# Performance work log

Hardware: AMD Instinct MI355X
Metric: run time of the kernel (lower is better)

## Reference

```python
import jax, jax.numpy as jnp
import numpy as np

B, C, H, W = 8, 256, 64, 64
NH = 8
CM = 2048
EPS = 1e-5


def setup_inputs() -> dict:
    key = jax.random.key(0)
    ks = jax.random.split(key, 16)
    n = lambda k, s: (jax.random.normal(k, s, dtype=jnp.float32) * 0.02)
    return {
        'x': jax.random.normal(ks[0], (B, C, H, W), dtype=jnp.float32),
        'Wqkv': n(ks[1], (C, 3 * C)), 'bqkv': n(ks[2], (3 * C,)),
        'dw_w': n(ks[3], (C, 1, 3, 3)), 'dw_b': n(ks[4], (C,)),
        'Wproj': n(ks[5], (C, C)), 'bproj': n(ks[6], (C,)),
        'bn1_g': jnp.ones((C,), jnp.float32), 'bn1_b': jnp.zeros((C,), jnp.float32),
        'bn1_m': n(ks[7], (C,)), 'bn1_v': jax.random.uniform(ks[8], (C,), dtype=jnp.float32) + 0.5,
        'alpha1': jnp.ones((1,), jnp.float32),
        'Wfc1': n(ks[9], (C, CM)), 'bfc1': n(ks[10], (CM,)),
        'Wfc2': n(ks[11], (CM, C)), 'bfc2': n(ks[12], (C,)),
        'bn2_g': jnp.ones((C,), jnp.float32), 'bn2_b': jnp.zeros((C,), jnp.float32),
        'bn2_m': n(ks[13], (C,)), 'bn2_v': jax.random.uniform(ks[14], (C,), dtype=jnp.float32) + 0.5,
        'alpha2': jnp.ones((1,), jnp.float32),
    }


def _repbn(x, g, b, m, v, alpha):
    # eval-mode RepBN: BatchNorm1d with running stats over channel dim + alpha*x
    bn = (x - m) * jax.lax.rsqrt(v + EPS) * g + b
    return bn + alpha * x


def reference(x, Wqkv, bqkv, dw_w, dw_b, Wproj, bproj,
              bn1_g, bn1_b, bn1_m, bn1_v, alpha1,
              Wfc1, bfc1, Wfc2, bfc2,
              bn2_g, bn2_b, bn2_m, bn2_v, alpha2):
    b, c, h, w = x.shape
    n = h * w
    hd = c // NH
    scale = hd ** (-0.5)
    t = x.reshape(b, c, n).transpose(0, 2, 1)  # [B,N,C]

    # --- SimplifiedLinearAttention ---
    qkv = (t @ Wqkv + bqkv).reshape(b, n, 3, NH, hd).transpose(2, 0, 3, 1, 4)
    q, k, v = qkv[0], qkv[1], qkv[2]          # [B,H,N,hd]
    q = jax.nn.relu(q) * scale
    k = jax.nn.relu(k)
    ctx = jnp.einsum('bhnd,bhne->bhde', k, v)  # [B,H,hd,hd] small context
    out = jnp.einsum('bhnd,bhde->bhne', q, ctx)
    out = out.transpose(0, 2, 1, 3).reshape(b, n, c)
    img = out.transpose(0, 2, 1).reshape(b, c, h, w)
    img = jax.lax.conv_general_dilated(img, dw_w, (1, 1), 'SAME',
                                       feature_group_count=c)
    img = img + dw_b[None, :, None, None]
    out = img.reshape(b, c, n).transpose(0, 2, 1)
    out = out @ Wproj + bproj

    # residual + RepBN (eval branch of LinearNorm)
    t = _repbn(t + out, bn1_g, bn1_b, bn1_m, bn1_v, alpha1)

    # FFN (exact GELU as nn.GELU default)
    ff = jax.nn.gelu(t @ Wfc1 + bfc1, approximate=False) @ Wfc2 + bfc2
    t = _repbn(t + ff, bn2_g, bn2_b, bn2_m, bn2_v, alpha2)

    return t.transpose(0, 2, 1).reshape(b, c, h, w)
```

## Files before the change

### kernel.cpp

```cpp
#include <hip/hip_runtime.h>
#include <hip/hip_bf16.h>
#include <math.h>

constexpr int B_ = 8, C_ = 256, H_ = 64, W_ = 64;
constexpr int N_ = H_ * W_;
constexpr int NH_ = 8;
constexpr int CM_ = 2048;
constexpr int M_ = B_ * N_;
constexpr float EPS_ = 1e-5f;

typedef __bf16 bf16_t;
typedef bf16_t bf16x4 __attribute__((ext_vector_type(4)));
typedef bf16_t bf16x8 __attribute__((ext_vector_type(8)));
typedef float f32x4 __attribute__((ext_vector_type(4)));

__device__ inline bf16_t f2b(float f) {
    __hip_bfloat16 h = __float2bfloat16(f);
    return *reinterpret_cast<bf16_t*>(&h);
}
__device__ inline float b2f(bf16_t b) {
    unsigned short u = *reinterpret_cast<unsigned short*>(&b);
    unsigned int x = (unsigned int)u << 16;
    return *reinterpret_cast<float*>(&x);
}
__device__ inline float gelu_ap(float y) {
    float u = y * (0.7978845608f + 0.0356774081f * y * y);
    float e = __expf(2.0f * u);
    return y - y * __builtin_amdgcn_rcpf(e + 1.0f);
}

#define GLOAD_LDS16(gptr, lptr)                                                     \
    __builtin_amdgcn_global_load_lds(                                               \
        (const __attribute__((address_space(1))) void*)(gptr),                      \
        (__attribute__((address_space(3))) void*)(lptr), 16, 0, 0)

template <int MODE>
__global__ void transpose_cast(const void* __restrict__ in_, bf16_t* __restrict__ outb) {
    __shared__ float tile[32][33];
    int b  = blockIdx.z;
    int n0 = blockIdx.x * 32;
    int c0 = blockIdx.y * 32;
    int tx = threadIdx.x, ty = threadIdx.y;
#pragma unroll
    for (int i = ty; i < 32; i += 8) {
        size_t off = (size_t)b * C_ * N_ + (size_t)(c0 + i) * N_ + n0 + tx;
        tile[i][tx] = (MODE == 0) ? ((const float*)in_)[off] : b2f(((const bf16_t*)in_)[off]);
    }
    __syncthreads();
#pragma unroll
    for (int i = ty; i < 32; i += 8) {
        size_t off = (size_t)b * N_ * C_ + (size_t)(n0 + i) * C_ + c0 + tx;
        outb[off] = f2b(tile[tx][i]);
    }
}

__global__ void wcastT(const float* __restrict__ W, bf16_t* __restrict__ Wt,
                       int K, int N) {
    __shared__ float tile[32][33];
    int k0 = blockIdx.y * 32, n0 = blockIdx.x * 32;
    int tx = threadIdx.x, ty = threadIdx.y;
#pragma unroll
    for (int i = ty; i < 32; i += 8)
        tile[i][tx] = W[(size_t)(k0 + i) * N + n0 + tx];
    __syncthreads();
#pragma unroll
    for (int i = ty; i < 32; i += 8)
        Wt[(size_t)(n0 + i) * K + k0 + tx] = f2b(tile[tx][i]);
}

template <int EPI>
__global__ __launch_bounds__(256)
void gemm_swp(const bf16_t* __restrict__ Wt, const bf16_t* __restrict__ Act,
              const float* __restrict__ bias, bf16_t* __restrict__ Cb,
              int M, int N, int K,
              const bf16_t* __restrict__ tres_b,
              const float* __restrict__ g, const float* __restrict__ bb,
              const float* __restrict__ mm, const float* __restrict__ vv,
              const float* __restrict__ alpha) {
    __shared__ bf16x8 ldsv[2048];
    char* lds = (char*)ldsv;

    int tid  = threadIdx.x;
    int lane = tid & 63;
    int w    = tid >> 6;
    int wi   = w >> 1, wj = w & 1;

    int nwg = gridDim.x * gridDim.y;
    int bid = blockIdx.y * gridDim.x + blockIdx.x;
    int swz = (bid & 7) * (nwg >> 3) + (bid >> 3);
    int bx = swz % gridDim.x, by = swz / gridDim.x;
    int bch = bx * 128, bm = by * 128;

    int rowl = lane & 15, kq = lane >> 4;

    f32x4 acc[4][4] = {};

    for (int k0 = 0; k0 < K; k0 += 64) {
#pragma unroll
        for (int j = 0; j < 4; ++j) {
            int jj = w * 4 + j;
            int msub = jj >> 1, kh = jj & 1;
            const bf16_t* gw = Wt + ((size_t)(bch + msub * 16 + rowl) * K + k0 + kh * 32 + kq * 8);
            GLOAD_LDS16(gw, lds + jj * 1024);
            const bf16_t* ga = Act + ((size_t)(bm + msub * 16 + rowl) * K + k0 + kh * 32 + kq * 8);
            GLOAD_LDS16(ga, lds + 16384 + jj * 1024);
        }
        __syncthreads();
#pragma unroll
        for (int ks = 0; ks < 2; ++ks) {
            bf16x8 wf[4], af[4];
#pragma unroll
            for (int i = 0; i < 4; ++i) wf[i] = ldsv[((wi * 4 + i) * 2 + ks) * 64 + lane];
#pragma unroll
            for (int j = 0; j < 4; ++j) af[j] = ldsv[1024 + ((wj * 4 + j) * 2 + ks) * 64 + lane];
#pragma unroll
            for (int i = 0; i < 4; ++i)
#pragma unroll
                for (int j = 0; j < 4; ++j)
                    acc[i][j] = __builtin_amdgcn_mfma_f32_16x16x32_bf16(wf[i], af[j], acc[i][j], 0, 0, 0);
        }
        __syncthreads();
    }

    float alpha_v = (EPI == 1) ? alpha[0] : 0.f;
#pragma unroll
    for (int i = 0; i < 4; ++i) {
        int ch = bch + wi * 64 + i * 16 + (lane >> 4) * 4;
        f32x4 b4 = *(const f32x4*)(bias + ch);
        f32x4 rs4, B4, m4;
        if (EPI == 1) {
            f32x4 g4 = *(const f32x4*)(g + ch);
            f32x4 v4 = *(const f32x4*)(vv + ch);
            B4 = *(const f32x4*)(bb + ch);
            m4 = *(const f32x4*)(mm + ch);
#pragma unroll
            for (int r = 0; r < 4; ++r) rs4[r] = rsqrtf(v4[r] + EPS_) * g4[r];
        }
#pragma unroll
        for (int j = 0; j < 4; ++j) {
            int m = bm + wj * 64 + j * 16 + (lane & 15);
            f32x4 a = acc[i][j];
            bf16_t ob[4];
            if (EPI == 4) {
#pragma unroll
                for (int r = 0; r < 4; ++r) ob[r] = f2b(a[r] + b4[r]);
            } else if (EPI == 2) {
#pragma unroll
                for (int r = 0; r < 4; ++r) ob[r] = f2b(gelu_ap(a[r] + b4[r]));
            } else {
                bf16x4 t4 = *(const bf16x4*)(tres_b + (size_t)m * N + ch);
#pragma unroll
                for (int r = 0; r < 4; ++r) {
                    float z = b2f(t4[r]) + a[r] + b4[r];
                    ob[r] = f2b((z - m4[r]) * rs4[r] + B4[r] + alpha_v * z);
                }
            }
            *(bf16x4*)(Cb + (size_t)m * N + ch) = *(bf16x4*)ob;
        }
    }
}

__global__ __launch_bounds__(256)
void gemm_bf16(const bf16_t* __restrict__ A, const bf16_t* __restrict__ Bt,
               const float* __restrict__ bias,
               float* __restrict__ Cf,
               int M, int N, int K,
               const bf16_t* __restrict__ tres_b,
               const float* __restrict__ g, const float* __restrict__ bb,
               const float* __restrict__ mm, const float* __restrict__ vv,
               const float* __restrict__ alpha) {
    __shared__ bf16x8 ldsv[2048];
    char* lds = (char*)ldsv;

    int tid  = threadIdx.x;
    int lane = tid & 63;
    int w    = tid >> 6;
    int wm   = w >> 1, wn = w & 1;

    int nwg = gridDim.x * gridDim.y;
    int bid = blockIdx.y * gridDim.x + blockIdx.x;
    int swz = (bid & 7) * (nwg >> 3) + (bid >> 3);
    int bx = swz % gridDim.x, by = swz / gridDim.x;
    int brow = by * 128, bcol = bx * 128;

    int rowl = lane & 15, kq = lane >> 4;

    f32x4 acc[4][4] = {};

    for (int k0 = 0; k0 < K; k0 += 64) {
#pragma unroll
        for (int j = 0; j < 4; ++j) {
            int jj = w * 4 + j;
            int msub = jj >> 1, kh = jj & 1;
            const bf16_t* ga = A + ((size_t)(brow + msub * 16 + rowl) * K + k0 + kh * 32 + kq * 8);
            GLOAD_LDS16(ga, lds + jj * 1024);
            const bf16_t* gb = Bt + ((size_t)(bcol + msub * 16 + rowl) * K + k0 + kh * 32 + kq * 8);
            GLOAD_LDS16(gb, lds + 16384 + jj * 1024);
        }
        __syncthreads();
#pragma unroll
        for (int ks = 0; ks < 2; ++ks) {
            bf16x8 af[4], bfr[4];
#pragma unroll
            for (int m = 0; m < 4; ++m) af[m] = ldsv[((wm * 4 + m) * 2 + ks) * 64 + lane];
#pragma unroll
            for (int n = 0; n < 4; ++n) bfr[n] = ldsv[1024 + ((wn * 4 + n) * 2 + ks) * 64 + lane];
#pragma unroll
            for (int m = 0; m < 4; ++m)
#pragma unroll
                for (int n = 0; n < 4; ++n)
                    acc[m][n] = __builtin_amdgcn_mfma_f32_16x16x32_bf16(af[m], bfr[n], acc[m][n], 0, 0, 0);
        }
        __syncthreads();
    }

    float alpha_v = alpha[0];
#pragma unroll
    for (int m = 0; m < 4; ++m) {
        int mbase = brow + wm * 64 + m * 16 + (lane >> 4) * 4;
        int bi = mbase >> 12, ni = mbase & (N_ - 1);
#pragma unroll
        for (int n = 0; n < 4; ++n) {
            int col = bcol + wn * 64 + n * 16 + (lane & 15);
            float bv = bias[col];
            float rs = rsqrtf(vv[col] + EPS_) * g[col];
            float bbv = bb[col], mv = mm[col];
            f32x4 o4;
#pragma unroll
            for (int r = 0; r < 4; ++r) {
                float z = b2f(tres_b[(size_t)(mbase + r) * C_ + col]) + acc[m][n][r] + bv;
                o4[r] = (z - mv) * rs + bbv + alpha_v * z;
            }
            *(f32x4*)(Cf + ((size_t)bi * C_ + col) * N_ + ni) = o4;
        }
    }
}

__global__ void ctx_partial(const bf16_t* __restrict__ qkv, float* __restrict__ ctxp) {
    __shared__ float kb[64][40];
    __shared__ float vb[64][40];
    int seg = blockIdx.x;
    int bh  = blockIdx.y;
    int b = bh >> 3, h = bh & 7;
    int tid = threadIdx.x;
    int d  = tid >> 3;
    int e0 = (tid & 7) * 4;
    int lrow = tid >> 2, lcol = (tid & 3) * 8;
    float acc[4] = {0.f, 0.f, 0.f, 0.f};
    const size_t base = (size_t)b * N_ * 768 + h * 32;
    for (int n0 = seg * 512; n0 < seg * 512 + 512; n0 += 64) {
        size_t ra = base + (size_t)(n0 + lrow) * 768 + lcol;
        bf16x8 kv8 = *(const bf16x8*)(qkv + ra + 256);
        bf16x8 vv8 = *(const bf16x8*)(qkv + ra + 512);
#pragma unroll
        for (int j = 0; j < 8; ++j) {
            kb[lrow][lcol + j] = b2f(kv8[j]);
            vb[lrow][lcol + j] = b2f(vv8[j]);
        }
        __syncthreads();
#pragma unroll
        for (int nl = 0; nl < 64; ++nl) {
            float kv = fmaxf(kb[nl][d], 0.f);
#pragma unroll
            for (int j = 0; j < 4; ++j)
                acc[j] = fmaf(kv, vb[nl][e0 + j], acc[j]);
        }
        __syncthreads();
    }
    float* o = ctxp + ((size_t)seg * 64 + bh) * 1024 + d * 32 + e0;
#pragma unroll
    for (int j = 0; j < 4; ++j) o[j] = acc[j];
}

__global__ void ctx_reduce(const float* __restrict__ ctxp, float* __restrict__ ctx) {
    int idx = blockIdx.x * 256 + threadIdx.x;
    float s = 0.f;
#pragma unroll
    for (int seg = 0; seg < 8; ++seg) s += ctxp[(size_t)seg * 65536 + idx];
    ctx[idx] = s;
}

__global__ void attn_out(const bf16_t* __restrict__ qkv, const float* __restrict__ ctx,
                         bf16_t* __restrict__ img) {
    __shared__ float qb[64][33];
    __shared__ float cs[32][32];
    int n0 = blockIdx.x * 64;
    int bh = blockIdx.y;
    int b = bh >> 3, h = bh & 7;
    int tid = threadIdx.x;
    const float scale = 0.17677669529663687f;
    {
        float4 vv = ((const float4*)(ctx + (size_t)bh * 1024))[tid];
        ((float4*)&cs[0][0])[tid] = vv;
    }
    const size_t base = (size_t)b * N_ * 768 + h * 32;
    int lrow = tid >> 2, lcol = (tid & 3) * 8;
    {
        bf16x8 q8 = *(const bf16x8*)(qkv + base + (size_t)(n0 + lrow) * 768 + lcol);
#pragma unroll
        for (int j = 0; j < 8; ++j)
            qb[lrow][lcol + j] = fmaxf(b2f(q8[j]), 0.f) * scale;
    }
    __syncthreads();
    int nl = tid & 63, ebase = tid >> 6;
    bf16_t* outp = img + ((size_t)b * C_ + h * 32) * N_ + n0 + nl;
#pragma unroll
    for (int p = 0; p < 8; ++p) {
        int e = ebase + p * 4;
        float s = 0.f;
#pragma unroll
        for (int dd = 0; dd < 32; ++dd)
            s = fmaf(qb[nl][dd], cs[dd][e], s);
        outp[(size_t)e * N_] = f2b(s);
    }
}

__global__ __launch_bounds__(256)
void dwconv3x3(const bf16_t* __restrict__ img, const float* __restrict__ w,
               const float* __restrict__ bias, bf16_t* __restrict__ out) {
    __shared__ float sp[64][65];
    int bc = blockIdx.x;
    int c  = bc & 255;
    int tid = threadIdx.x;
    const bf16_t* ip = img + (size_t)bc * N_;
#pragma unroll
    for (int l = 0; l < 2; ++l) {
        int flat = (tid + l * 256) * 8;
        int row = flat >> 6, col = flat & 63;
        bf16x8 v8 = *(const bf16x8*)(ip + flat);
#pragma unroll
        for (int j = 0; j < 8; ++j) sp[row][col + j] = b2f(v8[j]);
    }
    float wv[9];
#pragma unroll
    for (int j = 0; j < 9; ++j) wv[j] = w[c * 9 + j];
    float bv = bias[c];
    __syncthreads();

    int y = tid >> 2, x0 = (tid & 3) * 16;
    float o[16];
#pragma unroll
    for (int i = 0; i < 16; ++i) o[i] = bv;
#pragma unroll
    for (int dy = -1; dy <= 1; ++dy) {
        int yy = y + dy;
        if (yy < 0 || yy > 63) continue;
#pragma unroll
        for (int dx = -1; dx <= 1; ++dx) {
            float wgt = wv[(dy + 1) * 3 + dx + 1];
#pragma unroll
            for (int i = 0; i < 16; ++i) {
                int xx = x0 + i + dx;
                float val = (xx < 0 || xx > 63) ? 0.f : sp[yy][xx];
                o[i] = fmaf(wgt, val, o[i]);
            }
        }
    }
    bf16_t ob[16];
#pragma unroll
    for (int i = 0; i < 16; ++i) ob[i] = f2b(o[i]);
    *(bf16x8*)(out + (size_t)bc * N_ + y * 64 + x0)     = *(bf16x8*)&ob[0];
    *(bf16x8*)(out + (size_t)bc * N_ + y * 64 + x0 + 8) = *(bf16x8*)&ob[8];
}

extern "C" void kernel_launch(void* const* d_in, const int* in_sizes, int n_in,
                              void* d_out, int out_size, void* d_ws, size_t ws_size,
                              hipStream_t stream) {
    const float* x     = (const float*)d_in[0];
    const float* Wqkv  = (const float*)d_in[1];
    const float* bqkv  = (const float*)d_in[2];
    const float* dw_w  = (const float*)d_in[3];
    const float* dw_b  = (const float*)d_in[4];
    const float* Wproj = (const float*)d_in[5];
    const float* bproj = (const float*)d_in[6];
    const float* bn1_g = (const float*)d_in[7];
    const float* bn1_b = (const float*)d_in[8];
    const float* bn1_m = (const float*)d_in[9];
    const float* bn1_v = (const float*)d_in[10];
    const float* alpha1= (const float*)d_in[11];
    const float* Wfc1  = (const float*)d_in[12];
    const float* bfc1  = (const float*)d_in[13];
    const float* Wfc2  = (const float*)d_in[14];
    const float* bfc2  = (const float*)d_in[15];
    const float* bn2_g = (const float*)d_in[16];
    const float* bn2_b = (const float*)d_in[17];
    const float* bn2_m = (const float*)d_in[18];
    const float* bn2_v = (const float*)d_in[19];
    const float* alpha2= (const float*)d_in[20];
    float* out = (float*)d_out;

    char* ws = (char*)d_ws;
    bf16_t* t_b2    = (bf16_t*)(ws);
    bf16_t* WqkvT   = (bf16_t*)(ws + 16777216);
    bf16_t* WprojT  = (bf16_t*)(ws + 17170432);
    bf16_t* Wfc1T   = (bf16_t*)(ws + 17301504);
    bf16_t* Wfc2T   = (bf16_t*)(ws + 18350080);
    float*  ctxp    = (float*)(ws + 19398656);
    float*  ctx     = (float*)(ws + 21495808);
    bf16_t* t_b     = (bf16_t*)(ws + 21757952);
    bf16_t* qkv_b   = (bf16_t*)(ws + 38535168);
    bf16_t* img_b   = (bf16_t*)(ws + 88866816);
    bf16_t* conv_b  = (bf16_t*)(ws + 105644032);
    bf16_t* convT_b = (bf16_t*)(ws + 122421248);
    bf16_t* hidden  = (bf16_t*)(ws + 21757952);

    transpose_cast<0><<<dim3(N_ / 32, C_ / 32, B_), dim3(32, 8), 0, stream>>>(x, t_b);
    wcastT<<<dim3(768 / 32, C_ / 32), dim3(32, 8), 0, stream>>>(Wqkv, WqkvT, C_, 768);
    wcastT<<<dim3(C_ / 32, C_ / 32), dim3(32, 8), 0, stream>>>(Wproj, WprojT, C_, C_);
    wcastT<<<dim3(CM_ / 32, C_ / 32), dim3(32, 8), 0, stream>>>(Wfc1, Wfc1T, C_, CM_);
    wcastT<<<dim3(C_ / 32, CM_ / 32), dim3(32, 8), 0, stream>>>(Wfc2, Wfc2T, CM_, C_);

    gemm_swp<4><<<dim3(768 / 128, M_ / 128), 256, 0, stream>>>(
        WqkvT, t_b, bqkv, qkv_b, M_, 768, C_,
        nullptr, nullptr, nullptr, nullptr, nullptr, nullptr);

    ctx_partial<<<dim3(8, B_ * NH_), 256, 0, stream>>>(qkv_b, ctxp);
    ctx_reduce<<<256, 256, 0, stream>>>(ctxp, ctx);

    attn_out<<<dim3(N_ / 64, B_ * NH_), 256, 0, stream>>>(qkv_b, ctx, img_b);

    dwconv3x3<<<B_ * C_, 256, 0, stream>>>(img_b, dw_w, dw_b, conv_b);

    transpose_cast<1><<<dim3(N_ / 32, C_ / 32, B_), dim3(32, 8), 0, stream>>>(conv_b, convT_b);

    gemm_swp<1><<<dim3(C_ / 128, M_ / 128), 256, 0, stream>>>(
        WprojT, convT_b, bproj, t_b2, M_, C_, C_,
        t_b, bn1_g, bn1_b, bn1_m, bn1_v, alpha1);

    gemm_swp<2><<<dim3(CM_ / 128, M_ / 128), 256, 0, stream>>>(
        Wfc1T, t_b2, bfc1, hidden, M_, CM_, C_,
        nullptr, nullptr, nullptr, nullptr, nullptr, nullptr);

    gemm_bf16<<<dim3(C_ / 128, M_ / 128), 256, 0, stream>>>(
        hidden, Wfc2T, bfc2, out, M_, C_, CM_,
        t_b2, bn2_g, bn2_b, bn2_m, bn2_v, alpha2);
}
```

Measured before the change: 338.0 us.

## Double-buffer LDS in GEMM kernels and merge prep casts into one launch

Both GEMM kernels now use two LDS buffers, issuing async global-to-LDS loads for the next K tile while the MFMAs run on the current one. This drops one barrier per iteration. The input transpose and the four weight transpose-casts are merged into a single launch to cut launch overhead. In exchange, LDS per block doubles to 64KB, which may lower occupancy.

```diff
diff --git a/kernel.cpp b/kernel.cpp
--- a/kernel.cpp
+++ b/kernel.cpp
@@ -34,38 +34,57 @@
         (const __attribute__((address_space(1))) void*)(gptr),                      \
         (__attribute__((address_space(3))) void*)(lptr), 16, 0, 0)
 
-template <int MODE>
-__global__ void transpose_cast(const void* __restrict__ in_, bf16_t* __restrict__ outb) {
+__global__ __launch_bounds__(256)
+void prep(const float* __restrict__ x, bf16_t* __restrict__ t_b,
+          const float* __restrict__ Wqkv, bf16_t* __restrict__ WqkvT,
+          const float* __restrict__ Wproj, bf16_t* __restrict__ WprojT,
+          const float* __restrict__ Wfc1, bf16_t* __restrict__ Wfc1T,
+          const float* __restrict__ Wfc2, bf16_t* __restrict__ Wfc2T) {
     __shared__ float tile[32][33];
-    int b  = blockIdx.z;
-    int n0 = blockIdx.x * 32;
-    int c0 = blockIdx.y * 32;
+    int id = blockIdx.x;
     int tx = threadIdx.x, ty = threadIdx.y;
-#pragma unroll
-    for (int i = ty; i < 32; i += 8) {
-        size_t off = (size_t)b * C_ * N_ + (size_t)(c0 + i) * N_ + n0 + tx;
-        tile[i][tx] = (MODE == 0) ? ((const float*)in_)[off] : b2f(((const bf16_t*)in_)[off]);
-    }
-    __syncthreads();
-#pragma unroll
-    for (int i = ty; i < 32; i += 8) {
-        size_t off = (size_t)b * N_ * C_ + (size_t)(n0 + i) * C_ + c0 + tx;
-        outb[off] = f2b(tile[tx][i]);
-    }
-}
-
-__global__ void wcastT(const float* __restrict__ W, bf16_t* __restrict__ Wt,
-                       int K, int N) {
-    __shared__ float tile[32][33];
-    int k0 = blockIdx.y * 32, n0 = blockIdx.x * 32;
-    int tx = threadIdx.x, ty = threadIdx.y;
+
+    const float* src;
+    bf16_t* dst;
+    int K, N, k0, n0;
+    size_t soff, doff;
+
+    if (id < 8192) {
+        int b = id >> 10, rem = id & 1023;
+        int nn = (rem & 127) * 32, cc = (rem >> 7) * 32;
+        src = x; dst = t_b; K = 0; N = 0;
+#pragma unroll
+        for (int i = ty; i < 32; i += 8)
+            tile[i][tx] = x[(size_t)b * C_ * N_ + (size_t)(cc + i) * N_ + nn + tx];
+        __syncthreads();
+#pragma unroll
+        for (int i = ty; i < 32; i += 8)
+            t_b[(size_t)b * N_ * C_ + (size_t)(nn + i) * C_ + cc + tx] = f2b(tile[tx][i]);
+        return;
+    } else if (id < 8384) {
+        int idw = id - 8192; K = C_; N = 768;
+        n0 = (idw % 24) * 32; k0 = (idw / 24) * 32;
+        src = Wqkv; dst = WqkvT;
+    } else if (id < 8448) {
+        int idw = id - 8384; K = C_; N = C_;
+        n0 = (idw & 7) * 32; k0 = (idw >> 3) * 32;
+        src = Wproj; dst = WprojT;
+    } else if (id < 8960) {
+        int idw = id - 8448; K = C_; N = CM_;
+        n0 = (idw & 63) * 32; k0 = (idw >> 6) * 32;
+        src = Wfc1; dst = Wfc1T;
+    } else {
+        int idw = id - 8960; K = CM_; N = C_;
+        n0 = (idw & 7) * 32; k0 = (idw >> 3) * 32;
+        src = Wfc2; dst = Wfc2T;
+    }
 #pragma unroll
     for (int i = ty; i < 32; i += 8)
-        tile[i][tx] = W[(size_t)(k0 + i) * N + n0 + tx];
+        tile[i][tx] = src[(size_t)(k0 + i) * N + n0 + tx];
     __syncthreads();
 #pragma unroll
     for (int i = ty; i < 32; i += 8)
-        Wt[(size_t)(n0 + i) * K + k0 + tx] = f2b(tile[tx][i]);
+        dst[(size_t)(n0 + i) * K + k0 + tx] = f2b(tile[tx][i]);
 }
 
 template <int EPI>
@@ -77,7 +96,7 @@
               const float* __restrict__ g, const float* __restrict__ bb,
               const float* __restrict__ mm, const float* __restrict__ vv,
               const float* __restrict__ alpha) {
-    __shared__ bf16x8 ldsv[2048];
+    __shared__ bf16x8 ldsv[4096];
     char* lds = (char*)ldsv;
 
     int tid  = threadIdx.x;
@@ -93,33 +112,47 @@
 
     int rowl = lane & 15, kq = lane >> 4;
 
+    const bf16_t* wbase = Wt  + (size_t)(bch + (w >> 1) * 32) * K;
+    (void)wbase;
+
+#define STAGE_SWP(k0, p)                                                             \
+    {                                                                                \
+        _Pragma("unroll")                                                            \
+        for (int j = 0; j < 4; ++j) {                                                \
+            int jj = w * 4 + j;                                                      \
+            int msub = jj >> 1, kh = jj & 1;                                         \
+            const bf16_t* gw = Wt + ((size_t)(bch + msub * 16 + rowl) * K + (k0) +   \
+                                     kh * 32 + kq * 8);                              \
+            GLOAD_LDS16(gw, lds + (p) * 32768 + jj * 1024);                          \
+            const bf16_t* ga = Act + ((size_t)(bm + msub * 16 + rowl) * K + (k0) +   \
+                                      kh * 32 + kq * 8);                             \
+            GLOAD_LDS16(ga, lds + (p) * 32768 + 16384 + jj * 1024);                  \
+        }                                                                            \
+    }
+
     f32x4 acc[4][4] = {};
-
-    for (int k0 = 0; k0 < K; k0 += 64) {
-#pragma unroll
-        for (int j = 0; j < 4; ++j) {
-            int jj = w * 4 + j;
-            int msub = jj >> 1, kh = jj & 1;
-            const bf16_t* gw = Wt + ((size_t)(bch + msub * 16 + rowl) * K + k0 + kh * 32 + kq * 8);
-            GLOAD_LDS16(gw, lds + jj * 1024);
-            const bf16_t* ga = Act + ((size_t)(bm + msub * 16 + rowl) * K + k0 + kh * 32 + kq * 8);
-            GLOAD_LDS16(ga, lds + 16384 + jj * 1024);
-        }
-        __syncthreads();
+    int T = K >> 6;
+
+    STAGE_SWP(0, 0);
+    __syncthreads();
+
+    for (int t = 0; t < T; ++t) {
+        int p = t & 1;
+        if (t + 1 < T) STAGE_SWP((t + 1) << 6, p ^ 1);
 #pragma unroll
         for (int ks = 0; ks < 2; ++ks) {
             bf16x8 wf[4], af[4];
 #pragma unroll
-            for (int i = 0; i < 4; ++i) wf[i] = ldsv[((wi * 4 + i) * 2 + ks) * 64 + lane];
-#pragma unroll
-            for (int j = 0; j < 4; ++j) af[j] = ldsv[1024 + ((wj * 4 + j) * 2 + ks) * 64 + lane];
+            for (int i = 0; i < 4; ++i) wf[i] = ldsv[p * 2048 + ((wi * 4 + i) * 2 + ks) * 64 + lane];
+#pragma unroll
+            for (int j = 0; j < 4; ++j) af[j] = ldsv[p * 2048 + 1024 + ((wj * 4 + j) * 2 + ks) * 64 + lane];
 #pragma unroll
             for (int i = 0; i < 4; ++i)
 #pragma unroll
                 for (int j = 0; j < 4; ++j)
                     acc[i][j] = __builtin_amdgcn_mfma_f32_16x16x32_bf16(wf[i], af[j], acc[i][j], 0, 0, 0);
         }
-        __syncthreads();
+        if (t + 1 < T) __syncthreads();
     }
 
     float alpha_v = (EPI == 1) ? alpha[0] : 0.f;
@@ -169,7 +202,7 @@
                const float* __restrict__ g, const float* __restrict__ bb,
                const float* __restrict__ mm, const float* __restrict__ vv,
                const float* __restrict__ alpha) {
-    __shared__ bf16x8 ldsv[2048];
+    __shared__ bf16x8 ldsv[4096];
     char* lds = (char*)ldsv;
 
     int tid  = threadIdx.x;
@@ -185,33 +218,44 @@
 
     int rowl = lane & 15, kq = lane >> 4;
 
+#define STAGE_NSW(k0, p)                                                             \
+    {                                                                                \
+        _Pragma("unroll")                                                            \
+        for (int j = 0; j < 4; ++j) {                                                \
+            int jj = w * 4 + j;                                                      \
+            int msub = jj >> 1, kh = jj & 1;                                         \
+            const bf16_t* ga = A + ((size_t)(brow + msub * 16 + rowl) * K + (k0) +   \
+                                    kh * 32 + kq * 8);                               \
+            GLOAD_LDS16(ga, lds + (p) * 32768 + jj * 1024);                          \
+            const bf16_t* gb = Bt + ((size_t)(bcol + msub * 16 + rowl) * K + (k0) +  \
+                                     kh * 32 + kq * 8);                              \
+            GLOAD_LDS16(gb, lds + (p) * 32768 + 16384 + jj * 1024);                  \
+        }                                                                            \
+    }
+
     f32x4 acc[4][4] = {};
-
-    for (int k0 = 0; k0 < K; k0 += 64) {
-#pragma unroll
-        for (int j = 0; j < 4; ++j) {
-            int jj = w * 4 + j;
-            int msub = jj >> 1, kh = jj & 1;
-            const bf16_t* ga = A + ((size_t)(brow + msub * 16 + rowl) * K + k0 + kh * 32 + kq * 8);
-            GLOAD_LDS16(ga, lds + jj * 1024);
-            const bf16_t* gb = Bt + ((size_t)(bcol + msub * 16 + rowl) * K + k0 + kh * 32 + kq * 8);
-            GLOAD_LDS16(gb, lds + 16384 + jj * 1024);
-        }
-        __syncthreads();
+    int T = K >> 6;
+
+    STAGE_NSW(0, 0);
+    __syncthreads();
+
+    for (int t = 0; t < T; ++t) {
+        int p = t & 1;
+        if (t + 1 < T) STAGE_NSW((t + 1) << 6, p ^ 1);
 #pragma unroll
         for (int ks = 0; ks < 2; ++ks) {
             bf16x8 af[4], bfr[4];
 #pragma unroll
-            for (int m = 0; m < 4; ++m) af[m] = ldsv[((wm * 4 + m) * 2 + ks) * 64 + lane];
-#pragma unroll
-            for (int n = 0; n < 4; ++n) bfr[n] = ldsv[1024 + ((wn * 4 + n) * 2 + ks) * 64 + lane];
+            for (int m = 0; m < 4; ++m) af[m] = ldsv[p * 2048 + ((wm * 4 + m) * 2 + ks) * 64 + lane];
+#pragma unroll
+            for (int n = 0; n < 4; ++n) bfr[n] = ldsv[p * 2048 + 1024 + ((wn * 4 + n) * 2 + ks) * 64 + lane];
 #pragma unroll
             for (int m = 0; m < 4; ++m)
 #pragma unroll
                 for (int n = 0; n < 4; ++n)
                     acc[m][n] = __builtin_amdgcn_mfma_f32_16x16x32_bf16(af[m], bfr[n], acc[m][n], 0, 0, 0);
         }
-        __syncthreads();
+        if (t + 1 < T) __syncthreads();
     }
 
     float alpha_v = alpha[0];
@@ -234,6 +278,21 @@
             *(f32x4*)(Cf + ((size_t)bi * C_ + col) * N_ + ni) = o4;
         }
     }
+}
+
+__global__ void transpose_b(const bf16_t* __restrict__ in_, bf16_t* __restrict__ outb) {
+    __shared__ float tile[32][33];
+    int b  = blockIdx.z;
+    int n0 = blockIdx.x * 32;
+    int c0 = blockIdx.y * 32;
+    int tx = threadIdx.x, ty = threadIdx.y;
+#pragma unroll
+    for (int i = ty; i < 32; i += 8)
+        tile[i][tx] = b2f(in_[(size_t)b * C_ * N_ + (size_t)(c0 + i) * N_ + n0 + tx]);
+    __syncthreads();
+#pragma unroll
+    for (int i = ty; i < 32; i += 8)
+        outb[(size_t)b * N_ * C_ + (size_t)(n0 + i) * C_ + c0 + tx] = f2b(tile[tx][i]);
 }
 
 __global__ void ctx_partial(const bf16_t* __restrict__ qkv, float* __restrict__ ctxp) {
@@ -404,11 +463,8 @@
     bf16_t* convT_b = (bf16_t*)(ws + 122421248);
     bf16_t* hidden  = (bf16_t*)(ws + 21757952);
 
-    transpose_cast<0><<<dim3(N_ / 32, C_ / 32, B_), dim3(32, 8), 0, stream>>>(x, t_b);
-    wcastT<<<dim3(768 / 32, C_ / 32), dim3(32, 8), 0, stream>>>(Wqkv, WqkvT, C_, 768);
-    wcastT<<<dim3(C_ / 32, C_ / 32), dim3(32, 8), 0, stream>>>(Wproj, WprojT, C_, C_);
-    wcastT<<<dim3(CM_ / 32, C_ / 32), dim3(32, 8), 0, stream>>>(Wfc1, Wfc1T, C_, CM_);
-    wcastT<<<dim3(C_ / 32, CM_ / 32), dim3(32, 8), 0, stream>>>(Wfc2, Wfc2T, CM_, C_);
+    prep<<<9472, dim3(32, 8), 0, stream>>>(x, t_b, Wqkv, WqkvT, Wproj, WprojT,
+                                           Wfc1, Wfc1T, Wfc2, Wfc2T);
 
     gemm_swp<4><<<dim3(768 / 128, M_ / 128), 256, 0, stream>>>(
         WqkvT, t_b, bqkv, qkv_b, M_, 768, C_,
@@ -421,7 +477,7 @@
 
     dwconv3x3<<<B_ * C_, 256, 0, stream>>>(img_b, dw_w, dw_b, conv_b);
 
-    transpose_cast<1><<<dim3(N_ / 32, C_ / 32, B_), dim3(32, 8), 0, stream>>>(conv_b, convT_b);
+    transpose_b<<<dim3(N_ / 32, C_ / 32, B_), dim3(32, 8), 0, stream>>>(conv_b, convT_b);
 
     gemm_swp<1><<<dim3(C_ / 128, M_ / 128), 256, 0, stream>>>(
         WprojT, convT_b, bproj, t_b2, M_, C_, C_,
```

Result: no change. 332.2 us (-1.7%).
